# Kernel tuning notes

Measured on AMD Instinct MI355X. Metric: run time of the kernel, lower is better.

Reference implementation:

```python
import jax, jax.numpy as jnp
import numpy as np

EPS = 1e-6
B, S, D = 2, 2048, 2048
NH, NKV, HD = 16, 4, 128
DFF = 5632
WINDOW = 512


def rmsnorm(x, w):
    var = jnp.mean(x * x, axis=-1, keepdims=True)
    return x * jax.lax.rsqrt(var + EPS) * w


def rotate_half(x):
    x1, x2 = jnp.split(x, 2, axis=-1)
    return jnp.concatenate([-x2, x1], axis=-1)


def apply_rope(x, cos, sin):
    # x: (B, H, S, HD); cos/sin: (S, HD)
    return x * cos[None, None] + rotate_half(x) * sin[None, None]


def setup_inputs() -> dict:
    key = jax.random.key(0)
    ks = jax.random.split(key, 12)
    s = lambda n: (1.0 / np.sqrt(n))
    inp = {
        "hidden_states": jax.random.normal(ks[0], (B, S, D), jnp.float32),
        "cos": jnp.cos(jnp.arange(S)[:, None] / (10000.0 ** (jnp.concatenate([jnp.arange(HD // 2), jnp.arange(HD // 2)]) * 2.0 / HD))),
        "sin": jnp.sin(jnp.arange(S)[:, None] / (10000.0 ** (jnp.concatenate([jnp.arange(HD // 2), jnp.arange(HD // 2)]) * 2.0 / HD))),
        "ln1_w": jnp.ones((D,), jnp.float32),
        "ln2_w": jnp.ones((D,), jnp.float32),
        "wq": jax.random.normal(ks[1], (NH * HD, D), jnp.float32) * s(D),
        "wk": jax.random.normal(ks[2], (NKV * HD, D), jnp.float32) * s(D),
        "wv": jax.random.normal(ks[3], (NKV * HD, D), jnp.float32) * s(D),
        "wo": jax.random.normal(ks[4], (D, NH * HD), jnp.float32) * s(NH * HD),
        "w_gate": jax.random.normal(ks[5], (DFF, D), jnp.float32) * s(D),
        "w_up": jax.random.normal(ks[6], (DFF, D), jnp.float32) * s(D),
        "w_down": jax.random.normal(ks[7], (D, DFF), jnp.float32) * s(DFF),
    }
    return inp


def reference(hidden_states, cos, sin, ln1_w, ln2_w, wq, wk, wv, wo, w_gate, w_up, w_down):
    x = hidden_states
    # --- attention block ---
    h = rmsnorm(x, ln1_w)
    q = jnp.einsum("bsd,ed->bse", h, wq).reshape(B, S, NH, HD).transpose(0, 2, 1, 3)
    k = jnp.einsum("bsd,ed->bse", h, wk).reshape(B, S, NKV, HD).transpose(0, 2, 1, 3)
    v = jnp.einsum("bsd,ed->bse", h, wv).reshape(B, S, NKV, HD).transpose(0, 2, 1, 3)
    q = apply_rope(q, cos, sin)
    k = apply_rope(k, cos, sin)
    rep = NH // NKV
    k = jnp.repeat(k, rep, axis=1)  # (B, NH, S, HD)
    v = jnp.repeat(v, rep, axis=1)
    scale = 1.0 / np.sqrt(HD)
    scores = jnp.einsum("bhqd,bhkd->bhqk", q, k) * scale
    pos = jnp.arange(S)
    diff = pos[:, None] - pos[None, :]
    allowed = (diff >= 0) & (diff < WINDOW)  # causal + sliding window
    scores = jnp.where(allowed[None, None], scores, jnp.finfo(scores.dtype).min)
    attn = jax.nn.softmax(scores, axis=-1)
    out = jnp.einsum("bhqk,bhkd->bhqd", attn, v)
    out = out.transpose(0, 2, 1, 3).reshape(B, S, NH * HD)
    out = jnp.einsum("bse,de->bsd", out, wo)
    x = x + out
    # --- SwiGLU MLP block ---
    h = rmsnorm(x, ln2_w)
    gate = jax.nn.silu(jnp.einsum("bsd,fd->bsf", h, w_gate))
    up = jnp.einsum("bsd,fd->bsf", h, w_up)
    mlp = jnp.einsum("bsf,df->bsd", gate * up, w_down)
    return x + mlp
```

## Files before the change

kernel.cpp:

```cpp
#include <hip/hip_runtime.h>

typedef unsigned short u16;
typedef __attribute__((ext_vector_type(8))) short bf16x8;
typedef __attribute__((ext_vector_type(8))) unsigned short u16x8;
typedef __attribute__((ext_vector_type(4))) float f32x4;
typedef __attribute__((ext_vector_type(4))) _Float16 f16x4;

__device__ __forceinline__ u16 f2bf(float f) {
  union { float f; unsigned u; } v; v.f = f;
  unsigned r = v.u + 0x7fffu + ((v.u >> 16) & 1u);
  return (u16)(r >> 16);
}
__device__ __forceinline__ float bf2f(u16 u) {
  union { unsigned u; float f; } v; v.u = ((unsigned)u) << 16; return v.f;
}

#define GLOBAL_LOAD_LDS16(g, l)                                                \
  __builtin_amdgcn_global_load_lds(                                            \
      (const __attribute__((address_space(1))) void*)(g),                      \
      (__attribute__((address_space(3))) void*)(l), 16, 0, 0)

#define PHASE_TAIL()                                                           \
  asm volatile("s_waitcnt lgkmcnt(0)" ::: "memory");                           \
  __builtin_amdgcn_sched_barrier(0);                                           \
  __builtin_amdgcn_s_setprio(1)

__global__ __launch_bounds__(256) void rmsnorm_k(const float* __restrict__ x,
                                                 const float* __restrict__ w,
                                                 u16* __restrict__ out) {
  __shared__ float red[4];
  const int t = threadIdx.x;
  const size_t base = (size_t)blockIdx.x * 2048 + t * 8;
  float4 a = *(const float4*)(x + base);
  float4 b = *(const float4*)(x + base + 4);
  float ss = a.x * a.x + a.y * a.y + a.z * a.z + a.w * a.w +
             b.x * b.x + b.y * b.y + b.z * b.z + b.w * b.w;
#pragma unroll
  for (int o = 32; o; o >>= 1) ss += __shfl_xor(ss, o);
  if ((t & 63) == 0) red[t >> 6] = ss;
  __syncthreads();
  float rs = rsqrtf((red[0] + red[1] + red[2] + red[3]) * (1.0f / 2048.0f) + 1e-6f);
  float4 wa = *(const float4*)(w + t * 8);
  float4 wb = *(const float4*)(w + t * 8 + 4);
  u16x8 o8;
  o8[0] = f2bf(a.x * rs * wa.x); o8[1] = f2bf(a.y * rs * wa.y);
  o8[2] = f2bf(a.z * rs * wa.z); o8[3] = f2bf(a.w * rs * wa.w);
  o8[4] = f2bf(b.x * rs * wb.x); o8[5] = f2bf(b.y * rs * wb.y);
  o8[6] = f2bf(b.z * rs * wb.z); o8[7] = f2bf(b.w * rs * wb.w);
  *(u16x8*)(out + base) = o8;
}

__global__ __launch_bounds__(256) void rope_k(u16* __restrict__ buf,
                                              const float* __restrict__ cosp,
                                              const float* __restrict__ sinp,
                                              int nh, int total) {
  int i = blockIdx.x * 256 + threadIdx.x;
  if (i >= total) return;
  int d = i & 63;
  int hh = (i >> 6) % nh;
  int row = i / (64 * nh);
  int s = row & 2047;
  u16* p = buf + (size_t)row * (nh * 128) + hh * 128 + d;
  float x1 = bf2f(p[0]), x2 = bf2f(p[64]);
  float c1 = cosp[s * 128 + d], s1 = sinp[s * 128 + d];
  float c2 = cosp[s * 128 + d + 64], s2 = sinp[s * 128 + d + 64];
  p[0]  = f2bf(x1 * c1 - x2 * s1);
  p[64] = f2bf(x2 * c2 + x1 * s2);
}

__global__ __launch_bounds__(256) void rope_qkv(u16* __restrict__ buf,
                                                const float* __restrict__ cosp,
                                                const float* __restrict__ sinp) {
  int i = blockIdx.x * 256 + threadIdx.x;
  int d = i & 63;
  int hh = (i >> 6) % 20;
  int row = i / 1280;
  int s = row & 2047;
  int col = (hh < 16) ? hh * 128 + d : 2048 + (hh - 16) * 128 + d;
  u16* p = buf + (size_t)row * 3072 + col;
  float x1 = bf2f(p[0]), x2 = bf2f(p[64]);
  float c1 = cosp[s * 128 + d], s1 = sinp[s * 128 + d];
  float c2 = cosp[s * 128 + d + 64], s2 = sinp[s * 128 + d + 64];
  p[0]  = f2bf(x1 * c1 - x2 * s1);
  p[64] = f2bf(x2 * c2 + x1 * s2);
}

__global__ __launch_bounds__(256) void cvt_k(const float* __restrict__ s,
                                             u16* __restrict__ d, int n) {
  int stride = gridDim.x * 256 * 8;
  for (int i = (blockIdx.x * 256 + threadIdx.x) * 8; i < n; i += stride) {
    float4 a = *(const float4*)(s + i);
    float4 b = *(const float4*)(s + i + 4);
    u16x8 o;
    o[0] = f2bf(a.x); o[1] = f2bf(a.y); o[2] = f2bf(a.z); o[3] = f2bf(a.w);
    o[4] = f2bf(b.x); o[5] = f2bf(b.y); o[6] = f2bf(b.z); o[7] = f2bf(b.w);
    *(u16x8*)(d + i) = o;
  }
}

__global__ __launch_bounds__(256) void cvt3_k(const float* __restrict__ s0,
                                              const float* __restrict__ s1,
                                              const float* __restrict__ s2,
                                              u16* __restrict__ d,
                                              int n0, int n1, int n2) {
  int total = n0 + n1 + n2;
  int stride = gridDim.x * 256 * 8;
  for (int i = (blockIdx.x * 256 + threadIdx.x) * 8; i < total; i += stride) {
    const float* s; int off;
    if (i < n0)            { s = s0; off = i; }
    else if (i < n0 + n1)  { s = s1; off = i - n0; }
    else                   { s = s2; off = i - n0 - n1; }
    float4 a = *(const float4*)(s + off);
    float4 b = *(const float4*)(s + off + 4);
    u16x8 o;
    o[0] = f2bf(a.x); o[1] = f2bf(a.y); o[2] = f2bf(a.z); o[3] = f2bf(a.w);
    o[4] = f2bf(b.x); o[5] = f2bf(b.y); o[6] = f2bf(b.z); o[7] = f2bf(b.w);
    *(u16x8*)(d + i) = o;
  }
}

__device__ __forceinline__ void tile_swz(int bid, int nwg, int tm, int& bm, int& bn) {
  int cpx = nwg >> 3;
  int w = (bid & 7) * cpx + (bid >> 3);
  bm = w % tm;
  bn = w / tm;
}

template <int EPI>
__global__ __launch_bounds__(512, 2) void gemm2p(const u16* __restrict__ A,
                                                 const u16* __restrict__ Bw,
                                                 void* Cout, const float* resid,
                                                 int M, int N, int K) {
  const int NK = K >> 6;
  __shared__ u16 lds[73728];
  const int t = threadIdx.x, lane = t & 63, w = t >> 6;
  const int wm = w >> 2, wn = w & 3;
  const int l15 = lane & 15, lg = lane >> 4;
  int bm, bn;
  tile_swz(blockIdx.x, gridDim.x, M >> 7, bm, bn);

  const int r64 = t >> 3;
  const int gsrc = ((t & 7) ^ (r64 & 7)) * 8;
  const u16* Asrc[2];
#pragma unroll
  for (int u = 0; u < 2; ++u)
    Asrc[u] = A + (size_t)(bm * 128 + u * 64 + r64) * K + gsrc;
  const u16* Bsrc[4];
#pragma unroll
  for (int u = 0; u < 4; ++u)
    Bsrc[u] = Bw + (size_t)(bn * 256 + u * 64 + r64) * K + gsrc;
  const int d0 = t * 8;

#define STG_A2(buf, u, kt)                                                     \
  GLOBAL_LOAD_LDS16(Asrc[u] + (kt) * 64, &lds[(buf) * 24576 + (u) * 4096 + d0])
#define STG_B2(buf, u, kt)                                                     \
  GLOBAL_LOAD_LDS16(Bsrc[u] + (kt) * 64,                                       \
                    &lds[(buf) * 24576 + 8192 + (u) * 4096 + d0])

  const int swz0 = (lg ^ (l15 & 7)) * 8;
  const int swz1 = ((4 + lg) ^ (l15 & 7)) * 8;
  const int abase = wm * 4096 + l15 * 64;
  const int bbase = 8192 + wn * 4096 + l15 * 64;

  f32x4 acc[4][4] = {};
  bf16x8 af[4], bfr[4];

  STG_A2(0, 0, 0); STG_A2(0, 1, 0);
  STG_B2(0, 0, 0); STG_B2(0, 1, 0); STG_B2(0, 2, 0); STG_B2(0, 3, 0);
  STG_A2(1, 0, 1); STG_A2(1, 1, 1);
  STG_B2(1, 0, 1); STG_B2(1, 1, 1); STG_B2(1, 2, 1); STG_B2(1, 3, 1);
  asm volatile("s_waitcnt vmcnt(6)" ::: "memory");
  __builtin_amdgcn_s_barrier();

  for (int T = 0; T < NK; ++T) {
    const int bb = (T % 3) * 24576;
    const int nb = (T + 2) % 3;
#pragma unroll
    for (int i = 0; i < 4; ++i)
      af[i] = *(const bf16x8*)&lds[bb + abase + i * 1024 + swz0];
#pragma unroll
    for (int n = 0; n < 4; ++n)
      bfr[n] = *(const bf16x8*)&lds[bb + bbase + n * 1024 + swz0];
    if (T < NK - 2) { STG_A2(nb, 0, T + 2); STG_A2(nb, 1, T + 2); STG_B2(nb, 0, T + 2); }
    PHASE_TAIL();
#pragma unroll
    for (int i = 0; i < 4; ++i)
#pragma unroll
      for (int n = 0; n < 4; ++n)
        acc[i][n] = __builtin_amdgcn_mfma_f32_16x16x32_bf16(af[i], bfr[n], acc[i][n], 0, 0, 0);
    __builtin_amdgcn_s_setprio(0);
#pragma unroll
    for (int i = 0; i < 4; ++i)
      af[i] = *(const bf16x8*)&lds[bb + abase + i * 1024 + swz1];
#pragma unroll
    for (int n = 0; n < 4; ++n)
      bfr[n] = *(const bf16x8*)&lds[bb + bbase + n * 1024 + swz1];
    if (T < NK - 2) { STG_B2(nb, 1, T + 2); STG_B2(nb, 2, T + 2); STG_B2(nb, 3, T + 2); }
    PHASE_TAIL();
#pragma unroll
    for (int i = 0; i < 4; ++i)
#pragma unroll
      for (int n = 0; n < 4; ++n)
        acc[i][n] = __builtin_amdgcn_mfma_f32_16x16x32_bf16(af[i], bfr[n], acc[i][n], 0, 0, 0);
    __builtin_amdgcn_s_setprio(0);
    if (T < NK - 1) {
      if (T < NK - 2) asm volatile("s_waitcnt vmcnt(6)" ::: "memory");
      else            asm volatile("s_waitcnt vmcnt(0)" ::: "memory");
      __builtin_amdgcn_s_barrier();
    }
  }
#undef STG_A2
#undef STG_B2

#pragma unroll
  for (int mf = 0; mf < 4; ++mf)
#pragma unroll
    for (int nf = 0; nf < 4; ++nf)
#pragma unroll
      for (int r = 0; r < 4; ++r) {
        int row = bm * 128 + wm * 64 + mf * 16 + lg * 4 + r;
        int col = bn * 256 + wn * 64 + nf * 16 + l15;
        size_t idx = (size_t)row * N + col;
        if (EPI == 0)
          ((u16*)Cout)[idx] = f2bf(acc[mf][nf][r]);
        else
          ((float*)Cout)[idx] = resid[idx] + acc[mf][nf][r];
      }
}

__global__ __launch_bounds__(512, 2) void gu256(const u16* __restrict__ A,
                                                const u16* __restrict__ Wg,
                                                const u16* __restrict__ Wu,
                                                u16* __restrict__ G) {
  constexpr int KD = 2048, NK = 32;
  __shared__ u16 lds[65536];
  const int t = threadIdx.x, lane = t & 63, w = t >> 6;
  const int wm = w >> 2, wn = w & 3;
  const int l15 = lane & 15, lg = lane >> 4;
  int bm, bn;
  tile_swz(blockIdx.x, gridDim.x, 16, bm, bn);

  const int l8 = lane >> 3, g8 = lane & 7;
  const int gsrc = (g8 ^ l8) * 8;
  const u16* Asrc[2][2];
#pragma unroll
  for (int ha = 0; ha < 2; ++ha)
#pragma unroll
    for (int c = 0; c < 2; ++c)
      Asrc[ha][c] = A + (size_t)(bm * 256 + ha * 128 + w * 16 + c * 8 + l8) * KD + gsrc;
  const u16* Wsel = ((w >> 1) & 1) ? Wu : Wg;
  const u16* Bsrc[2][2];
#pragma unroll
  for (int hb = 0; hb < 2; ++hb)
#pragma unroll
    for (int c = 0; c < 2; ++c)
      Bsrc[hb][c] = Wsel + (size_t)(bn * 128 + (hb * 2 + (w >> 2)) * 32 +
                                    (w & 1) * 16 + c * 8 + l8) * KD + gsrc;
  const int dst_wl = w * 1024 + lane * 8;

#define STG_A(buf, ha, kt) do {                                                \
    GLOBAL_LOAD_LDS16(Asrc[ha][0] + (kt) * 64,                                 \
                      &lds[(buf) * 32768 + (ha) * 8192 + dst_wl]);             \
    GLOBAL_LOAD_LDS16(Asrc[ha][1] + (kt) * 64,                                 \
                      &lds[(buf) * 32768 + (ha) * 8192 + dst_wl + 512]); } while (0)
#define STG_B(buf, hb, kt) do {                                                \
    GLOBAL_LOAD_LDS16(Bsrc[hb][0] + (kt) * 64,                                 \
                      &lds[(buf) * 32768 + 16384 + (hb) * 8192 + dst_wl]);     \
    GLOBAL_LOAD_LDS16(Bsrc[hb][1] + (kt) * 64,                                 \
                      &lds[(buf) * 32768 + 16384 + (hb) * 8192 + dst_wl + 512]); } while (0)

  const int swz0 = (lg ^ (l15 & 7)) * 8;
  const int swz1 = ((4 + lg) ^ (l15 & 7)) * 8;
  const int abase = (wm * 128 + l15) * 64;
  const int bbase = 16384 + (wn * 64 + l15) * 64;

  f32x4 acc[8][4] = {};
  bf16x8 af[4], bf0[4], bf1[4];

  STG_A(0, 0, 0); STG_A(0, 1, 0);
  STG_B(0, 0, 0); STG_B(0, 1, 0);
  STG_B(1, 0, 1); STG_B(1, 1, 1);
  asm volatile("s_waitcnt vmcnt(4)" ::: "memory");
  __builtin_amdgcn_s_barrier();

  for (int T = 0; T < NK; ++T) {
    const int bb = (T & 1) * 32768;
    const int nbuf = (T + 1) & 1, cbuf = T & 1;
#pragma unroll
    for (int i = 0; i < 4; ++i)
      af[i] = *(const bf16x8*)&lds[bb + abase + i * 1024 + swz0];
#pragma unroll
    for (int n = 0; n < 4; ++n)
      bf0[n] = *(const bf16x8*)&lds[bb + bbase + n * 1024 + swz0];
    if (T < NK - 1) STG_A(nbuf, 0, T + 1);
    PHASE_TAIL();
#pragma unroll
    for (int i = 0; i < 4; ++i)
#pragma unroll
      for (int n = 0; n < 4; ++n)
        acc[i][n] = __builtin_amdgcn_mfma_f32_16x16x32_bf16(af[i], bf0[n], acc[i][n], 0, 0, 0);
    __builtin_amdgcn_s_setprio(0);
    __builtin_amdgcn_s_barrier();
#pragma unroll
    for (int i = 0; i < 4; ++i)
      af[i] = *(const bf16x8*)&lds[bb + abase + i * 1024 + swz1];
#pragma unroll
    for (int n = 0; n < 4; ++n)
      bf1[n] = *(const bf16x8*)&lds[bb + bbase + n * 1024 + swz1];
    if (T < NK - 1) STG_A(nbuf, 1, T + 1);
    PHASE_TAIL();
#pragma unroll
    for (int i = 0; i < 4; ++i)
#pragma unroll
      for (int n = 0; n < 4; ++n)
        acc[i][n] = __builtin_amdgcn_mfma_f32_16x16x32_bf16(af[i], bf1[n], acc[i][n], 0, 0, 0);
    __builtin_amdgcn_s_setprio(0);
    __builtin_amdgcn_s_barrier();
#pragma unroll
    for (int i = 0; i < 4; ++i)
      af[i] = *(const bf16x8*)&lds[bb + abase + (4 + i) * 1024 + swz0];
    if (T < NK - 2) STG_B(cbuf, 0, T + 2);
    PHASE_TAIL();
#pragma unroll
    for (int i = 0; i < 4; ++i)
#pragma unroll
      for (int n = 0; n < 4; ++n)
        acc[4 + i][n] = __builtin_amdgcn_mfma_f32_16x16x32_bf16(af[i], bf0[n], acc[4 + i][n], 0, 0, 0);
    __builtin_amdgcn_s_setprio(0);
    __builtin_amdgcn_s_barrier();
#pragma unroll
    for (int i = 0; i < 4; ++i)
      af[i] = *(const bf16x8*)&lds[bb + abase + (4 + i) * 1024 + swz1];
    if (T < NK - 2) STG_B(cbuf, 1, T + 2);
    PHASE_TAIL();
#pragma unroll
    for (int i = 0; i < 4; ++i)
#pragma unroll
      for (int n = 0; n < 4; ++n)
        acc[4 + i][n] = __builtin_amdgcn_mfma_f32_16x16x32_bf16(af[i], bf1[n], acc[4 + i][n], 0, 0, 0);
    __builtin_amdgcn_s_setprio(0);
    if (T < NK - 2) asm volatile("s_waitcnt vmcnt(4)" ::: "memory");
    else            asm volatile("s_waitcnt vmcnt(0)" ::: "memory");
    __builtin_amdgcn_s_barrier();
  }
#undef STG_A
#undef STG_B

  const size_t grow0 = (size_t)(bm * 256 + wm * 128 + lg * 4);
  const int gcol0 = bn * 128 + wn * 32 + l15;
#pragma unroll
  for (int mf = 0; mf < 8; ++mf)
#pragma unroll
    for (int p = 0; p < 2; ++p)
#pragma unroll
      for (int r = 0; r < 4; ++r) {
        float gg = acc[mf][p][r], uu = acc[mf][p + 2][r];
        float sg = gg / (1.0f + __expf(-gg));
        G[(grow0 + mf * 16 + r) * 5632 + gcol0 + p * 16] = f2bf(sg * uu);
      }
}

template <int EPI>
__global__ __launch_bounds__(256) void gemm_bt(const u16* __restrict__ A,
                                               const float* __restrict__ Bw,
                                               void* Cout, const float* resid,
                                               int M, int N, int K) {
  __shared__ u16 sA[128 * 32];
  __shared__ u16 sB[128 * 40];
  const int t = threadIdx.x, lane = t & 63, w = t >> 6;
  const int l15 = lane & 15, lg = lane >> 4;
  const int tn = N >> 7;
  const int bm = blockIdx.x / tn, bn = blockIdx.x % tn;
  const int wr = (w >> 1) << 6, wc = (w & 1) << 6;

  const u16* Ag  = A + (size_t)(bm * 128 + (t >> 2)) * K + (t & 3) * 8;
  const u16* Ag2 = Ag + (size_t)64 * K;
  const float* Bg  = Bw + (size_t)(bn * 128 + (t >> 2)) * K + (t & 3) * 8;
  const float* Bg2 = Bg + (size_t)64 * K;
  u16* sBp  = &sB[(t >> 2) * 40 + (t & 3) * 8];
  u16* sBp2 = sBp + 64 * 40;

  f32x4 acc[4][4] = {};

  for (int kt = 0; kt < K; kt += 32) {
    float4 b0 = *(const float4*)(Bg + kt);
    float4 b1 = *(const float4*)(Bg + kt + 4);
    float4 c0 = *(const float4*)(Bg2 + kt);
    float4 c1 = *(const float4*)(Bg2 + kt + 4);
    GLOBAL_LOAD_LDS16(Ag + kt, &sA[t * 8]);
    GLOBAL_LOAD_LDS16(Ag2 + kt, &sA[64 * 32 + t * 8]);
    u16x8 bs;
    bs[0] = f2bf(b0.x); bs[1] = f2bf(b0.y); bs[2] = f2bf(b0.z); bs[3] = f2bf(b0.w);
    bs[4] = f2bf(b1.x); bs[5] = f2bf(b1.y); bs[6] = f2bf(b1.z); bs[7] = f2bf(b1.w);
    *(u16x8*)sBp = bs;
    bs[0] = f2bf(c0.x); bs[1] = f2bf(c0.y); bs[2] = f2bf(c0.z); bs[3] = f2bf(c0.w);
    bs[4] = f2bf(c1.x); bs[5] = f2bf(c1.y); bs[6] = f2bf(c1.z); bs[7] = f2bf(c1.w);
    *(u16x8*)sBp2 = bs;
    __syncthreads();
    bf16x8 af[4], bfr[4];
#pragma unroll
    for (int m = 0; m < 4; ++m)
      af[m] = *(const bf16x8*)&sA[(wr + m * 16 + l15) * 32 + lg * 8];
#pragma unroll
    for (int n = 0; n < 4; ++n)
      bfr[n] = *(const bf16x8*)&sB[(wc + n * 16 + l15) * 40 + lg * 8];
#pragma unroll
    for (int m = 0; m < 4; ++m)
#pragma unroll
      for (int n = 0; n < 4; ++n)
        acc[m][n] = __builtin_amdgcn_mfma_f32_16x16x32_bf16(af[m], bfr[n], acc[m][n], 0, 0, 0);
    __syncthreads();
  }
#pragma unroll
  for (int m = 0; m < 4; ++m)
#pragma unroll
    for (int n = 0; n < 4; ++n)
#pragma unroll
      for (int r = 0; r < 4; ++r) {
        int row = bm * 128 + wr + m * 16 + lg * 4 + r;
        int col = bn * 128 + wc + n * 16 + l15;
        size_t idx = (size_t)row * N + col;
        if (EPI == 0)
          ((u16*)Cout)[idx] = f2bf(acc[m][n][r]);
        else
          ((float*)Cout)[idx] = resid[idx] + acc[m][n][r];
      }
}

__global__ __launch_bounds__(512) void gemm_gateup(const u16* __restrict__ A,
                                                   const float* __restrict__ Wg,
                                                   const float* __restrict__ Wu,
                                                   u16* __restrict__ G) {
  constexpr int N = 5632, K = 2048;
  __shared__ u16 sA[128 * 32];
  __shared__ u16 sB1[128 * 40];
  __shared__ u16 sB2[128 * 40];
  const int t = threadIdx.x, lane = t & 63, w = t >> 6;
  const int l15 = lane & 15, lg = lane >> 4;
  const int bm = blockIdx.x / 44, bn = blockIdx.x % 44;
  const int wr = (w >> 2) << 6, wc = (w & 3) << 5;

  const u16* Ag = A + (size_t)(bm * 128 + (t >> 2)) * K + (t & 3) * 8;
  const float* Bg1 = Wg + (size_t)(bn * 128 + (t >> 2)) * K + (t & 3) * 8;
  const float* Bg2 = Wu + (size_t)(bn * 128 + (t >> 2)) * K + (t & 3) * 8;
  const int sboff = (t >> 2) * 40 + (t & 3) * 8;

  f32x4 acc1[4][2] = {};
  f32x4 acc2[4][2] = {};

  for (int kt = 0; kt < K; kt += 32) {
    float4 g0 = *(const float4*)(Bg1 + kt);
    float4 g1 = *(const float4*)(Bg1 + kt + 4);
    float4 u0 = *(const float4*)(Bg2 + kt);
    float4 u1 = *(const float4*)(Bg2 + kt + 4);
    GLOBAL_LOAD_LDS16(Ag + kt, &sA[t * 8]);
    u16x8 bs;
    bs[0] = f2bf(g0.x); bs[1] = f2bf(g0.y); bs[2] = f2bf(g0.z); bs[3] = f2bf(g0.w);
    bs[4] = f2bf(g1.x); bs[5] = f2bf(g1.y); bs[6] = f2bf(g1.z); bs[7] = f2bf(g1.w);
    *(u16x8*)&sB1[sboff] = bs;
    bs[0] = f2bf(u0.x); bs[1] = f2bf(u0.y); bs[2] = f2bf(u0.z); bs[3] = f2bf(u0.w);
    bs[4] = f2bf(u1.x); bs[5] = f2bf(u1.y); bs[6] = f2bf(u1.z); bs[7] = f2bf(u1.w);
    *(u16x8*)&sB2[sboff] = bs;
    __syncthreads();
    bf16x8 af[4], b1f[2], b2f[2];
#pragma unroll
    for (int m = 0; m < 4; ++m)
      af[m] = *(const bf16x8*)&sA[(wr + m * 16 + l15) * 32 + lg * 8];
#pragma unroll
    for (int n = 0; n < 2; ++n) {
      b1f[n] = *(const bf16x8*)&sB1[(wc + n * 16 + l15) * 40 + lg * 8];
      b2f[n] = *(const bf16x8*)&sB2[(wc + n * 16 + l15) * 40 + lg * 8];
    }
#pragma unroll
    for (int m = 0; m < 4; ++m)
#pragma unroll
      for (int n = 0; n < 2; ++n) {
        acc1[m][n] = __builtin_amdgcn_mfma_f32_16x16x32_bf16(af[m], b1f[n], acc1[m][n], 0, 0, 0);
        acc2[m][n] = __builtin_amdgcn_mfma_f32_16x16x32_bf16(af[m], b2f[n], acc2[m][n], 0, 0, 0);
      }
    __syncthreads();
  }
#pragma unroll
  for (int m = 0; m < 4; ++m)
#pragma unroll
    for (int n = 0; n < 2; ++n)
#pragma unroll
      for (int r = 0; r < 4; ++r) {
        int row = bm * 128 + wr + m * 16 + lg * 4 + r;
        int col = bn * 128 + wc + n * 16 + l15;
        float ga = acc1[m][n][r], uu = acc2[m][n][r];
        float sg = ga / (1.0f + __expf(-ga));
        G[(size_t)row * N + col] = f2bf(sg * uu);
      }
}

__global__ __launch_bounds__(256) void attn_k(const u16* __restrict__ Q,
                                              const u16* __restrict__ K,
                                              const u16* __restrict__ V,
                                              u16* __restrict__ O,
                                              int qstr, int kvstr) {
  const int lane = threadIdx.x & 63;
  const int wid = blockIdx.x * 4 + (threadIdx.x >> 6);
  const int qt = wid & 127;
  const int h = (wid >> 7) & 15;
  const int b = wid >> 11;
  const int q0 = qt << 4;
  const int kvh = h >> 2;
  const int l15 = lane & 15, lg = lane >> 4;

  bf16x8 qf[4];
  {
    const u16* qp = Q + (size_t)((b << 11) + q0 + l15) * qstr + h * 128 + lg * 8;
#pragma unroll
    for (int ds = 0; ds < 4; ++ds) qf[ds] = *(const bf16x8*)(qp + ds * 32);
  }
  float m_run = -1e30f, l_run = 0.0f;
  f32x4 oacc[8];
#pragma unroll
  for (int db = 0; db < 8; ++db) oacc[db] = f32x4{0.f, 0.f, 0.f, 0.f};

  int lo = q0 - 511;
  if (lo < 0) lo = 0;
  for (int kb = (lo & ~15); kb <= q0; kb += 16) {
    f32x4 st = {0.f, 0.f, 0.f, 0.f};
    const u16* kp = K + (size_t)((b << 11) + kb + l15) * kvstr + kvh * 128 + lg * 8;
#pragma unroll
    for (int ds = 0; ds < 4; ++ds)
      st = __builtin_amdgcn_mfma_f32_16x16x32_bf16(*(const bf16x8*)(kp + ds * 32),
                                                   qf[ds], st, 0, 0, 0);
    const int qpos = q0 + l15;
    float pe[4];
    float tmax = -1e30f;
#pragma unroll
    for (int r = 0; r < 4; ++r) {
      int j = kb + lg * 4 + r;
      int d = qpos - j;
      bool ok = (d >= 0) && (d < 512);
      pe[r] = ok ? st[r] * 0.08838834764831845f : -1e30f;
      tmax = fmaxf(tmax, pe[r]);
    }
    tmax = fmaxf(tmax, __shfl_xor(tmax, 16));
    tmax = fmaxf(tmax, __shfl_xor(tmax, 32));
    float m_new = fmaxf(m_run, tmax);
    float corr = __expf(m_run - m_new);
    float psum = 0.0f;
#pragma unroll
    for (int r = 0; r < 4; ++r) {
      float e = (pe[r] > -1e29f) ? __expf(pe[r] - m_new) : 0.0f;
      pe[r] = e;
      psum += e;
    }
    psum += __shfl_xor(psum, 16);
    psum += __shfl_xor(psum, 32);
    l_run = l_run * corr + psum;
    m_run = m_new;

    f16x4 pf;
#pragma unroll
    for (int r = 0; r < 4; ++r) pf[r] = (_Float16)pe[r];

    float f0 = __shfl(corr, lg * 4 + 0);
    float f1 = __shfl(corr, lg * 4 + 1);
    float f2 = __shfl(corr, lg * 4 + 2);
    float f3 = __shfl(corr, lg * 4 + 3);
    const u16* vp = V + (size_t)((b << 11) + kb + lg * 4) * kvstr + kvh * 128 + l15;
#pragma unroll
    for (int db = 0; db < 8; ++db) {
      oacc[db][0] *= f0; oacc[db][1] *= f1; oacc[db][2] *= f2; oacc[db][3] *= f3;
      f16x4 vf;
#pragma unroll
      for (int e = 0; e < 4; ++e)
        vf[e] = (_Float16)bf2f(vp[(size_t)e * kvstr + db * 16]);
      oacc[db] = __builtin_amdgcn_mfma_f32_16x16x16f16(pf, vf, oacc[db], 0, 0, 0);
    }
  }
  float inv = 1.0f / l_run;
  float g0 = __shfl(inv, lg * 4 + 0);
  float g1 = __shfl(inv, lg * 4 + 1);
  float g2 = __shfl(inv, lg * 4 + 2);
  float g3 = __shfl(inv, lg * 4 + 3);
  u16* op = O + (size_t)((b << 11) + q0 + lg * 4) * 2048 + h * 128 + l15;
#pragma unroll
  for (int db = 0; db < 8; ++db) {
    op[0 * 2048 + db * 16] = f2bf(oacc[db][0] * g0);
    op[1 * 2048 + db * 16] = f2bf(oacc[db][1] * g1);
    op[2 * 2048 + db * 16] = f2bf(oacc[db][2] * g2);
    op[3 * 2048 + db * 16] = f2bf(oacc[db][3] * g3);
  }
}

extern "C" void kernel_launch(void* const* d_in, const int* in_sizes, int n_in,
                              void* d_out, int out_size, void* d_ws, size_t ws_size,
                              hipStream_t stream) {
  const float* x    = (const float*)d_in[0];
  const float* cosp = (const float*)d_in[1];
  const float* sinp = (const float*)d_in[2];
  const float* ln1  = (const float*)d_in[3];
  const float* ln2  = (const float*)d_in[4];
  const float* wq   = (const float*)d_in[5];
  const float* wk   = (const float*)d_in[6];
  const float* wv   = (const float*)d_in[7];
  const float* wo   = (const float*)d_in[8];
  const float* wg   = (const float*)d_in[9];
  const float* wu   = (const float*)d_in[10];
  const float* wd   = (const float*)d_in[11];
  float* out = (float*)d_out;

  const size_t SZ_HQ  = 8388608;
  const size_t SZ_KV  = 2097152;
  const size_t SZ_QKV = 12582912;
  const size_t SZ_G   = 23068672;
  const size_t SZ_WB  = 23068672;
  const size_t need_old = (SZ_HQ * 3 + SZ_KV * 2 + SZ_G) * 2;
  const size_t need_new = (SZ_HQ * 2 + SZ_QKV + SZ_G + SZ_WB) * 2;
  if (ws_size < need_old) return;

  if (ws_size >= need_new) {
    u16* h   = (u16*)d_ws;
    u16* qkv = h + SZ_HQ;
    u16* at  = qkv + SZ_QKV;
    u16* g   = at + SZ_HQ;
    u16* wb  = g + SZ_G;
    u16* wqb = wb;
    u16* wob = wb;
    u16* wgb = wb;
    u16* wdb = wb;

    rmsnorm_k<<<4096, 256, 0, stream>>>(x, ln1, h);
    cvt3_k<<<2048, 256, 0, stream>>>(wq, wk, wv, wqb, 4194304, 1048576, 1048576);
    gemm2p<0><<<384, 512, 0, stream>>>(h, wqb, qkv, nullptr, 4096, 3072, 2048);
    rope_qkv<<<20480, 256, 0, stream>>>(qkv, cosp, sinp);
    attn_k<<<1024, 256, 0, stream>>>(qkv, qkv + 2048, qkv + 2560, at, 3072, 3072);
    cvt_k<<<2048, 256, 0, stream>>>(wo, wob, 4194304);
    gemm2p<1><<<256, 512, 0, stream>>>(at, wob, d_out, x, 4096, 2048, 2048);
    rmsnorm_k<<<4096, 256, 0, stream>>>(out, ln2, h);
    cvt3_k<<<2048, 256, 0, stream>>>(wg, wu, wu, wgb, 11534336, 11534336, 0);
    gu256<<<704, 512, 0, stream>>>(h, wgb, wgb + 11534336, g);
    cvt_k<<<2048, 256, 0, stream>>>(wd, wdb, 11534336);
    gemm2p<1><<<256, 512, 0, stream>>>(g, wdb, d_out, out, 4096, 2048, 5632);
  } else {
    u16* h  = (u16*)d_ws;
    u16* q  = h + SZ_HQ;
    u16* kk = q + SZ_HQ;
    u16* vv = kk + SZ_KV;
    u16* at = vv + SZ_KV;
    u16* g  = at + SZ_HQ;

    rmsnorm_k<<<4096, 256, 0, stream>>>(x, ln1, h);
    gemm_bt<0><<<512, 256, 0, stream>>>(h, wq, q,  nullptr, 4096, 2048, 2048);
    gemm_bt<0><<<128, 256, 0, stream>>>(h, wk, kk, nullptr, 4096, 512, 2048);
    gemm_bt<0><<<128, 256, 0, stream>>>(h, wv, vv, nullptr, 4096, 512, 2048);
    rope_k<<<16384, 256, 0, stream>>>(q, cosp, sinp, 16, 4194304);
    rope_k<<<4096, 256, 0, stream>>>(kk, cosp, sinp, 4, 1048576);
    attn_k<<<1024, 256, 0, stream>>>(q, kk, vv, at, 2048, 512);
    gemm_bt<1><<<512, 256, 0, stream>>>(at, wo, d_out, x, 4096, 2048, 2048);
    rmsnorm_k<<<4096, 256, 0, stream>>>(out, ln2, h);
    gemm_gateup<<<1408, 512, 0, stream>>>(h, wg, wu, g);
    gemm_bt<1><<<512, 256, 0, stream>>>(g, wd, d_out, out, 4096, 2048, 5632);
  }
}
```

Baseline: 570.1 us.

## Restructure gate/up GEMM to 128x128 tiles with triple-buffered LDS pipeline

Replaces the 256-row gate/up GEMM kernel with a 128x128 tile variant that uses a three-stage LDS ring buffer, prefetching two k-steps ahead and dropping the intra-iteration barriers. The grid doubles to 1408 blocks and the swizzle group width changes. The aim is more load/compute overlap and better wave balance across CUs. In exchange, each block has half the A-tile reuse per weight load, uses more LDS per block, and keeps fewer accumulators per wave.

```diff
diff --git a/kernel.cpp b/kernel.cpp
--- a/kernel.cpp
+++ b/kernel.cpp
@@ -228,135 +228,103 @@
       }
 }
 
-__global__ __launch_bounds__(512, 2) void gu256(const u16* __restrict__ A,
-                                                const u16* __restrict__ Wg,
-                                                const u16* __restrict__ Wu,
-                                                u16* __restrict__ G) {
-  constexpr int KD = 2048, NK = 32;
-  __shared__ u16 lds[65536];
+__global__ __launch_bounds__(512, 2) void gateup2p(const u16* __restrict__ A,
+                                                   const u16* __restrict__ Wg,
+                                                   const u16* __restrict__ Wu,
+                                                   u16* __restrict__ G) {
+  constexpr int K = 2048, NK = 32;
+  __shared__ u16 lds[73728];
   const int t = threadIdx.x, lane = t & 63, w = t >> 6;
   const int wm = w >> 2, wn = w & 3;
   const int l15 = lane & 15, lg = lane >> 4;
   int bm, bn;
-  tile_swz(blockIdx.x, gridDim.x, 16, bm, bn);
-
-  const int l8 = lane >> 3, g8 = lane & 7;
-  const int gsrc = (g8 ^ l8) * 8;
-  const u16* Asrc[2][2];
-#pragma unroll
-  for (int ha = 0; ha < 2; ++ha)
-#pragma unroll
-    for (int c = 0; c < 2; ++c)
-      Asrc[ha][c] = A + (size_t)(bm * 256 + ha * 128 + w * 16 + c * 8 + l8) * KD + gsrc;
-  const u16* Wsel = ((w >> 1) & 1) ? Wu : Wg;
-  const u16* Bsrc[2][2];
-#pragma unroll
-  for (int hb = 0; hb < 2; ++hb)
-#pragma unroll
-    for (int c = 0; c < 2; ++c)
-      Bsrc[hb][c] = Wsel + (size_t)(bn * 128 + (hb * 2 + (w >> 2)) * 32 +
-                                    (w & 1) * 16 + c * 8 + l8) * KD + gsrc;
-  const int dst_wl = w * 1024 + lane * 8;
-
-#define STG_A(buf, ha, kt) do {                                                \
-    GLOBAL_LOAD_LDS16(Asrc[ha][0] + (kt) * 64,                                 \
-                      &lds[(buf) * 32768 + (ha) * 8192 + dst_wl]);             \
-    GLOBAL_LOAD_LDS16(Asrc[ha][1] + (kt) * 64,                                 \
-                      &lds[(buf) * 32768 + (ha) * 8192 + dst_wl + 512]); } while (0)
-#define STG_B(buf, hb, kt) do {                                                \
-    GLOBAL_LOAD_LDS16(Bsrc[hb][0] + (kt) * 64,                                 \
-                      &lds[(buf) * 32768 + 16384 + (hb) * 8192 + dst_wl]);     \
-    GLOBAL_LOAD_LDS16(Bsrc[hb][1] + (kt) * 64,                                 \
-                      &lds[(buf) * 32768 + 16384 + (hb) * 8192 + dst_wl + 512]); } while (0)
+  tile_swz(blockIdx.x, gridDim.x, 32, bm, bn);
+
+  const int r64 = t >> 3;
+  const int gsrc = ((t & 7) ^ (r64 & 7)) * 8;
+  const u16* Asrc[2];
+#pragma unroll
+  for (int u = 0; u < 2; ++u)
+    Asrc[u] = A + (size_t)(bm * 128 + u * 64 + r64) * K + gsrc;
+  const u16* Wsel = (r64 < 32) ? Wg : Wu;
+  const u16* Bsrc[4];
+#pragma unroll
+  for (int u = 0; u < 4; ++u)
+    Bsrc[u] = Wsel + (size_t)(bn * 128 + u * 32 + (r64 & 31)) * K + gsrc;
+  const int d0 = t * 8;
+
+#define STG_A2(buf, u, kt)                                                     \
+  GLOBAL_LOAD_LDS16(Asrc[u] + (kt) * 64, &lds[(buf) * 24576 + (u) * 4096 + d0])
+#define STG_B2(buf, u, kt)                                                     \
+  GLOBAL_LOAD_LDS16(Bsrc[u] + (kt) * 64,                                       \
+                    &lds[(buf) * 24576 + 8192 + (u) * 4096 + d0])
 
   const int swz0 = (lg ^ (l15 & 7)) * 8;
   const int swz1 = ((4 + lg) ^ (l15 & 7)) * 8;
-  const int abase = (wm * 128 + l15) * 64;
-  const int bbase = 16384 + (wn * 64 + l15) * 64;
-
-  f32x4 acc[8][4] = {};
-  bf16x8 af[4], bf0[4], bf1[4];
-
-  STG_A(0, 0, 0); STG_A(0, 1, 0);
-  STG_B(0, 0, 0); STG_B(0, 1, 0);
-  STG_B(1, 0, 1); STG_B(1, 1, 1);
-  asm volatile("s_waitcnt vmcnt(4)" ::: "memory");
+  const int abase = wm * 4096 + l15 * 64;
+  const int bbase = 8192 + wn * 4096 + l15 * 64;
+
+  f32x4 acc[4][4] = {};
+  bf16x8 af[4], bfr[4];
+
+  STG_A2(0, 0, 0); STG_A2(0, 1, 0);
+  STG_B2(0, 0, 0); STG_B2(0, 1, 0); STG_B2(0, 2, 0); STG_B2(0, 3, 0);
+  STG_A2(1, 0, 1); STG_A2(1, 1, 1);
+  STG_B2(1, 0, 1); STG_B2(1, 1, 1); STG_B2(1, 2, 1); STG_B2(1, 3, 1);
+  asm volatile("s_waitcnt vmcnt(6)" ::: "memory");
   __builtin_amdgcn_s_barrier();
 
   for (int T = 0; T < NK; ++T) {
-    const int bb = (T & 1) * 32768;
-    const int nbuf = (T + 1) & 1, cbuf = T & 1;
+    const int bb = (T % 3) * 24576;
+    const int nb = (T + 2) % 3;
 #pragma unroll
     for (int i = 0; i < 4; ++i)
       af[i] = *(const bf16x8*)&lds[bb + abase + i * 1024 + swz0];
 #pragma unroll
     for (int n = 0; n < 4; ++n)
-      bf0[n] = *(const bf16x8*)&lds[bb + bbase + n * 1024 + swz0];
-    if (T < NK - 1) STG_A(nbuf, 0, T + 1);
+      bfr[n] = *(const bf16x8*)&lds[bb + bbase + n * 1024 + swz0];
+    if (T < NK - 2) { STG_A2(nb, 0, T + 2); STG_A2(nb, 1, T + 2); STG_B2(nb, 0, T + 2); }
     PHASE_TAIL();
 #pragma unroll
     for (int i = 0; i < 4; ++i)
 #pragma unroll
       for (int n = 0; n < 4; ++n)
-        acc[i][n] = __builtin_amdgcn_mfma_f32_16x16x32_bf16(af[i], bf0[n], acc[i][n], 0, 0, 0);
+        acc[i][n] = __builtin_amdgcn_mfma_f32_16x16x32_bf16(af[i], bfr[n], acc[i][n], 0, 0, 0);
     __builtin_amdgcn_s_setprio(0);
-    __builtin_amdgcn_s_barrier();
 #pragma unroll
     for (int i = 0; i < 4; ++i)
       af[i] = *(const bf16x8*)&lds[bb + abase + i * 1024 + swz1];
 #pragma unroll
     for (int n = 0; n < 4; ++n)
-      bf1[n] = *(const bf16x8*)&lds[bb + bbase + n * 1024 + swz1];
-    if (T < NK - 1) STG_A(nbuf, 1, T + 1);
+      bfr[n] = *(const bf16x8*)&lds[bb + bbase + n * 1024 + swz1];
+    if (T < NK - 2) { STG_B2(nb, 1, T + 2); STG_B2(nb, 2, T + 2); STG_B2(nb, 3, T + 2); }
     PHASE_TAIL();
 #pragma unroll
     for (int i = 0; i < 4; ++i)
 #pragma unroll
       for (int n = 0; n < 4; ++n)
-        acc[i][n] = __builtin_amdgcn_mfma_f32_16x16x32_bf16(af[i], bf1[n], acc[i][n], 0, 0, 0);
+        acc[i][n] = __builtin_amdgcn_mfma_f32_16x16x32_bf16(af[i], bfr[n], acc[i][n], 0, 0, 0);
     __builtin_amdgcn_s_setprio(0);
-    __builtin_amdgcn_s_barrier();
-#pragma unroll
-    for (int i = 0; i < 4; ++i)
-      af[i] = *(const bf16x8*)&lds[bb + abase + (4 + i) * 1024 + swz0];
-    if (T < NK - 2) STG_B(cbuf, 0, T + 2);
-    PHASE_TAIL();
-#pragma unroll
-    for (int i = 0; i < 4; ++i)
-#pragma unroll
-      for (int n = 0; n < 4; ++n)
-        acc[4 + i][n] = __builtin_amdgcn_mfma_f32_16x16x32_bf16(af[i], bf0[n], acc[4 + i][n], 0, 0, 0);
-    __builtin_amdgcn_s_setprio(0);
-    __builtin_amdgcn_s_barrier();
-#pragma unroll
-    for (int i = 0; i < 4; ++i)
-      af[i] = *(const bf16x8*)&lds[bb + abase + (4 + i) * 1024 + swz1];
-    if (T < NK - 2) STG_B(cbuf, 1, T + 2);
-    PHASE_TAIL();
-#pragma unroll
-    for (int i = 0; i < 4; ++i)
-#pragma unroll
-      for (int n = 0; n < 4; ++n)
-        acc[4 + i][n] = __builtin_amdgcn_mfma_f32_16x16x32_bf16(af[i], bf1[n], acc[4 + i][n], 0, 0, 0);
-    __builtin_amdgcn_s_setprio(0);
-    if (T < NK - 2) asm volatile("s_waitcnt vmcnt(4)" ::: "memory");
-    else            asm volatile("s_waitcnt vmcnt(0)" ::: "memory");
-    __builtin_amdgcn_s_barrier();
-  }
-#undef STG_A
-#undef STG_B
-
-  const size_t grow0 = (size_t)(bm * 256 + wm * 128 + lg * 4);
-  const int gcol0 = bn * 128 + wn * 32 + l15;
-#pragma unroll
-  for (int mf = 0; mf < 8; ++mf)
+    if (T < NK - 1) {
+      if (T < NK - 2) asm volatile("s_waitcnt vmcnt(6)" ::: "memory");
+      else            asm volatile("s_waitcnt vmcnt(0)" ::: "memory");
+      __builtin_amdgcn_s_barrier();
+    }
+  }
+#undef STG_A2
+#undef STG_B2
+
+#pragma unroll
+  for (int mf = 0; mf < 4; ++mf)
 #pragma unroll
     for (int p = 0; p < 2; ++p)
 #pragma unroll
       for (int r = 0; r < 4; ++r) {
         float gg = acc[mf][p][r], uu = acc[mf][p + 2][r];
         float sg = gg / (1.0f + __expf(-gg));
-        G[(grow0 + mf * 16 + r) * 5632 + gcol0 + p * 16] = f2bf(sg * uu);
+        int row = bm * 128 + wm * 64 + mf * 16 + lg * 4 + r;
+        int col = bn * 128 + wn * 32 + p * 16 + l15;
+        G[(size_t)row * 5632 + col] = f2bf(sg * uu);
       }
 }
 
@@ -635,7 +603,7 @@
     gemm2p<1><<<256, 512, 0, stream>>>(at, wob, d_out, x, 4096, 2048, 2048);
     rmsnorm_k<<<4096, 256, 0, stream>>>(out, ln2, h);
     cvt3_k<<<2048, 256, 0, stream>>>(wg, wu, wu, wgb, 11534336, 11534336, 0);
-    gu256<<<704, 512, 0, stream>>>(h, wgb, wgb + 11534336, g);
+    gateup2p<<<1408, 512, 0, stream>>>(h, wgb, wgb + 11534336, g);
     cvt_k<<<2048, 256, 0, stream>>>(wd, wdb, 11534336);
     gemm2p<1><<<256, 512, 0, stream>>>(g, wdb, d_out, out, 4096, 2048, 5632);
   } else {
```

Measured after the change: 586.1 us. 1.03x slower.
